# Kernel tuning notes

Measured on AMD Instinct MI355X. Metric: run time of the kernel, lower is better.

## Reference

```python
import jax, jax.numpy as jnp
import numpy as np

# LIDIA core constants (arch_opt.rgb=True => patch_w=5, k=14)
PS = 5          # patch width
K = 14          # number of nearest neighbors
WS = 15         # spatial search window (forward default is 29; 15 keeps working set in ridge regime)
SW = WS // 2    # search radius
PW = PS // 2    # patch radius
RAD = SW + PW   # total reflect pad


def setup_inputs() -> dict:
    key = jax.random.key(0)
    noisy = jax.random.uniform(key, (4, 3, 128, 128), dtype=jnp.float32) * 255.0
    sigma = jnp.full((1,), 25.0, dtype=jnp.float32)  # noise std on 0-255 scale
    return {"noisy": noisy, "sigma": sigma}


def reference(noisy, sigma):
    t, c, h, w = noisy.shape
    # rescale to [-1,1] and remove per-frame means (as in forward)
    x = (noisy / 255.0 - 0.5) / 0.5
    means = x.mean((-2, -1), keepdims=True)
    x = x - means

    # reflect pad so every search offset + patch stays in bounds
    P = jnp.pad(x, ((0, 0), (0, 0), (RAD, RAD), (RAD, RAD)), mode="reflect")
    Hp, Wp = h + 2 * PW, w + 2 * PW
    base = P[:, :, SW:SW + Hp, SW:SW + Wp]  # [t,c,Hp,Wp]

    # --- patch-kNN search: L2 patch distance for every offset in WSxWS window ---
    offs = jnp.stack(jnp.meshgrid(jnp.arange(WS), jnp.arange(WS), indexing="ij"),
                     axis=-1).reshape(-1, 2)  # [WS*WS, 2]

    def energy(o):
        sh = jax.lax.dynamic_slice(P, (0, 0, o[0], o[1]), (t, c, Hp, Wp))
        return ((base - sh) ** 2).sum(1)  # [t,Hp,Wp]

    E = jax.vmap(energy)(offs)  # [WS*WS, t, Hp, Wp] pixel-wise sq diffs

    # box-filter (PSxPS patch sum) -> per-center patch distances
    ones_k = jnp.ones((1, 1, PS, PS), dtype=E.dtype)
    D = jax.lax.conv_general_dilated(E.reshape(-1, 1, Hp, Wp), ones_k,
                                     window_strides=(1, 1), padding="VALID")
    D = D.reshape(WS * WS, t, h, w).transpose(1, 2, 3, 0)  # [t,h,w,WS*WS]

    # top-k smallest distances per query pixel
    negD, idx = jax.lax.top_k(-D, K)  # [t,h,w,K]
    topd = -negD
    oy = idx // WS  # offset row in [0,WS)
    ox = idx % WS

    # --- gather neighbor patches (irregular gather) ---
    # patch top-left in padded coords: row = i + oy  (RAD - SW - PW == 0)
    ii = jnp.arange(h)[None, :, None, None]
    jj = jnp.arange(w)[None, None, :, None]
    r0 = ii + oy  # [t,h,w,K]
    c0 = jj + ox
    a = jnp.arange(PS)
    rows = r0[..., None, None] + a[None, None, None, None, :, None]  # [t,h,w,K,PS,1]
    cols = c0[..., None, None] + a[None, None, None, None, None, :]  # [t,h,w,K,1,PS]
    tt = jnp.arange(t)[:, None, None, None, None, None]
    Pt = P.transpose(0, 2, 3, 1)  # [t,Hpad,Wpad,c]
    patches = Pt[tt, rows, cols]  # [t,h,w,K,PS,PS,c]

    # --- denoise: distance-based softmax aggregation over neighbors ---
    sig = sigma[0] / 255.0 / 0.5  # noise std in normalized units
    denom = 2.0 * (c * PS * PS) * (sig * sig) + 1e-8
    wts = jax.nn.softmax(-topd / denom, axis=-1)  # [t,h,w,K]
    deno_p = jnp.einsum("thwk,thwkpqc->thwpqc", wts, patches)  # [t,h,w,PS,PS,c]

    # --- fold: scatter-add overlapping denoised patches + counts ---
    rf = (jnp.arange(h)[:, None, None, None] + a[None, None, :, None])  # [h,1,PS,1]
    cf = (jnp.arange(w)[None, :, None, None] + a[None, None, None, :])  # [1,w,1,PS]
    tf = jnp.arange(t)[:, None, None, None, None]
    acc = jnp.zeros((t, Hp, Wp, c), dtype=deno_p.dtype)
    cnt = jnp.zeros((t, Hp, Wp, 1), dtype=deno_p.dtype)
    acc = acc.at[tf, rf[None], cf[None]].add(deno_p)
    cnt = cnt.at[tf, rf[None], cf[None]].add(
        jnp.ones((t, h, w, PS, PS, 1), dtype=deno_p.dtype))

    deno = acc / (cnt + 1e-10)
    deno = deno[:, PW:PW + h, PW:PW + w, :].transpose(0, 3, 1, 2)  # [t,c,h,w]
    deno = deno + means
    deno = 255.0 * (deno * 0.5 + 0.5)
    return deno
```

## Files before the change

### kernel.cpp

```cpp
#include <hip/hip_runtime.h>

#define T_ 4
#define C_ 3
#define H_ 128
#define W_ 128
#define PS_ 5
#define K_ 14
#define WS_ 15
#define SW_ 7
#define PW_ 2
#define RAD_ 9
#define HP_ 146
#define NOFF 225
#define NPIX (T_*H_*W_)
#define NQ 2

#define TILE 16
#define SPR 34
#define SPS 35
#define SSR 30
#define SSS 33
#define OB 23
#define CSOG 324

#define AT 8
#define APR 22
#define APS 23
#define AWR 12
#define AWS 20

typedef unsigned int u32;

__device__ __forceinline__ float4 load_refl(const float* __restrict__ noisy,
                                            int t, int py, int px) {
    int ry = py - RAD_; if (ry < 0) ry = -ry; if (ry > H_-1) ry = 2*(H_-1) - ry;
    int rx = px - RAD_; if (rx < 0) rx = -rx; if (rx > W_-1) rx = 2*(W_-1) - rx;
    const float* nt = noisy + (size_t)t*(C_*H_*W_) + ry*W_ + rx;
    float4 v;
    v.x = nt[0]          * (1.0f/127.5f) - 1.0f;
    v.y = nt[H_*W_]      * (1.0f/127.5f) - 1.0f;
    v.z = nt[2*(H_*W_)]  * (1.0f/127.5f) - 1.0f;
    v.w = 0.f;
    return v;
}

__global__ __launch_bounds__(512, 4) void fused_topk(const float* __restrict__ noisy,
                                                     uint4* __restrict__ pkey) {
    __shared__ __align__(16) float4 sP[SPR*SPS];
    __shared__ __align__(16) float  sS[SSR*SSS];
    __shared__ __align__(16) float  cs[OB*CSOG];

    const int tid = threadIdx.x;
    const int pix = tid & 255;
    const int part = tid >> 8;
    const int tx = pix & 15, ty = pix >> 4;
    const int z = blockIdx.z;
    const int t = z >> 1, q = z & 1;
    const int i0 = blockIdx.y * TILE, j0 = blockIdx.x * TILE;

    {
        float* qsq = cs;
        for (int e = tid; e < SPR*SPR; e += 512) {
            int r = e / SPR, c = e % SPR;
            float4 v = load_refl(noisy, t, i0 + r, j0 + c);
            sP[r*SPS + c] = v;
            qsq[r*35 + c] = v.x*v.x + v.y*v.y + v.z*v.z;
        }
    }
    __syncthreads();

    {
        const float* qsq = cs;
        float* cq  = cs + 1200;
        for (int e = tid; e < 30*34; e += 512) {
            int r = e / 34, c = e - r*34;
            const float* qp = &qsq[r*35 + c];
            cq[r*35 + c] = qp[0] + qp[35] + qp[70] + qp[105] + qp[140];
        }
        __syncthreads();
        for (int e = tid; e < 30*30; e += 512) {
            int r = e / 30, c = e - r*30;
            const float* cp = &cq[r*35 + c];
            sS[r*SSS + c] = cp[0] + cp[1] + cp[2] + cp[3] + cp[4];
        }
        __syncthreads();
    }

    const float Sbase = sS[(ty + SW_)*SSS + (tx + SW_)];

    const int og = tid / 20;
    const int cc = tid - og*20;
    const bool p1act = (tid < OB*20);
    float bx[20], by[20], bz[20];
    if (p1act) {
        #pragma unroll
        for (int r = 0; r < 20; ++r) {
            float4 v = sP[(SW_ + r)*SPS + (cc + SW_)];
            bx[r] = v.x; by[r] = v.y; bz[r] = v.z;
        }
    }
    float* myv = &cs[og*CSOG + cc];

    const int p2o = tid >> 4;
    const int p2i = tid & 15;
    float* p2row = &cs[p2o*CSOG + p2i*20];

    const float* vb = &cs[ty*20 + tx];

    u32 kb[K_];
    #pragma unroll
    for (int k = 0; k < K_; ++k) kb[k] = 0xFFFFFFFFu;

    const int obeg = q ? 113 : 0;
    const int oend = q ? 225 : 113;
    const int nb = (oend - obeg + OB - 1) / OB;

    for (int bi = 0; bi < nb; ++bi) {
        const int ob = (q == 0) ? (obeg + (nb - 1 - bi)*OB) : (obeg + bi*OB);
        int o = ob + og;
        if (p1act && o < oend) {
            u32 oyu = (u32)o / 15u, oxu = (u32)o - oyu*15u;
            const float4* sp = &sP[(int)oyu*SPS + cc + (int)oxu];
            float ring[5]; float run = 0.f;
            #pragma unroll
            for (int r = 0; r < 20; ++r) {
                float4 sv = sp[r*SPS];
                float hr = bx[r]*sv.x + by[r]*sv.y + bz[r]*sv.z;
                if (r < 5) run += hr;
                else       run += hr - ring[r % 5];
                ring[r % 5] = hr;
                if (r >= 4) myv[(r-4)*20] = run;
            }
        }
        __syncthreads();
        if (p2o < OB && (ob + p2o) < oend) {
            float4 A = *(const float4*)(p2row);
            float4 B = *(const float4*)(p2row + 4);
            float4 Cv = *(const float4*)(p2row + 8);
            float4 Dv = *(const float4*)(p2row + 12);
            float4 Ev = *(const float4*)(p2row + 16);
            float v0=A.x,v1=A.y,v2=A.z,v3=A.w,v4=B.x,v5=B.y,v6=B.z,v7=B.w;
            float v8=Cv.x,v9=Cv.y,v10=Cv.z,v11=Cv.w,v12=Dv.x,v13=Dv.y,v14=Dv.z,v15=Dv.w;
            float v16=Ev.x,v17=Ev.y,v18=Ev.z,v19=Ev.w;
            float r0 = v0+v1+v2+v3+v4;
            float r1 = r0 + v5 - v0;
            float r2 = r1 + v6 - v1;
            float r3 = r2 + v7 - v2;
            float r4 = r3 + v8 - v3;
            float r5 = r4 + v9 - v4;
            float r6 = r5 + v10 - v5;
            float r7 = r6 + v11 - v6;
            float r8 = r7 + v12 - v7;
            float r9 = r8 + v13 - v8;
            float r10 = r9 + v14 - v9;
            float r11 = r10 + v15 - v10;
            float r12 = r11 + v16 - v11;
            float r13 = r12 + v17 - v12;
            float r14 = r13 + v18 - v13;
            float r15 = r14 + v19 - v14;
            *(float4*)(p2row)      = make_float4(r0, r1, r2, r3);
            *(float4*)(p2row + 4)  = make_float4(r4, r5, r6, r7);
            *(float4*)(p2row + 8)  = make_float4(r8, r9, r10, r11);
            *(float4*)(p2row + 12) = make_float4(r12, r13, r14, r15);
        }
        __syncthreads();
        for (int g = part; g < OB; g += 2) {
            int o2 = ob + g;
            if (o2 >= oend) break;
            u32 oy2 = (u32)o2 / 15u, ox2 = (u32)o2 - oy2*15u;
            float V = vb[g*CSOG];
            float d = fmaxf(Sbase + sS[(ty + (int)oy2)*SSS + (tx + (int)ox2)] - 2.f*V, 0.f);
            u32 c = (__float_as_uint(d) & 0xFFFFFF00u) | (u32)o2;
            #pragma unroll
            for (int k = K_-1; k > 0; --k) kb[k] = min(kb[k], max(kb[k-1], c));
            kb[0] = min(kb[0], c);
        }
        __syncthreads();
    }

    if (part == 1) {
        u32* ex = (u32*)cs + pix*20;
        *(uint4*)(ex)      = make_uint4(kb[0],  kb[1],  kb[2],  kb[3]);
        *(uint4*)(ex + 4)  = make_uint4(kb[4],  kb[5],  kb[6],  kb[7]);
        *(uint4*)(ex + 8)  = make_uint4(kb[8],  kb[9],  kb[10], kb[11]);
        *(uint4*)(ex + 12) = make_uint4(kb[12], kb[13], 0xFFFFFFFFu, 0xFFFFFFFFu);
    }
    __syncthreads();
    if (part == 0) {
        const u32* ex = (const u32*)cs + pix*20;
        uint4 e0 = *(const uint4*)(ex);
        uint4 e1 = *(const uint4*)(ex + 4);
        uint4 e2 = *(const uint4*)(ex + 8);
        uint4 e3 = *(const uint4*)(ex + 12);
        u32 A[16] = {kb[0],kb[1],kb[2],kb[3],kb[4],kb[5],kb[6],kb[7],
                     kb[8],kb[9],kb[10],kb[11],kb[12],kb[13],0xFFFFFFFFu,0xFFFFFFFFu};
        u32 B[16] = {e0.x,e0.y,e0.z,e0.w, e1.x,e1.y,e1.z,e1.w,
                     e2.x,e2.y,e2.z,e2.w, e3.x,e3.y,e3.z,e3.w};
        #pragma unroll
        for (int i2 = 0; i2 < 16; ++i2) A[i2] = min(A[i2], B[15 - i2]);
        #define CEX(x,y) { u32 mn = min(A[x],A[y]); u32 mx = max(A[x],A[y]); A[x]=mn; A[y]=mx; }
        CEX(0,8) CEX(1,9) CEX(2,10) CEX(3,11) CEX(4,12) CEX(5,13) CEX(6,14) CEX(7,15)
        CEX(0,4) CEX(1,5) CEX(2,6) CEX(3,7) CEX(8,12) CEX(9,13) CEX(10,14) CEX(11,15)
        CEX(0,2) CEX(1,3) CEX(4,6) CEX(5,7) CEX(8,10) CEX(9,11) CEX(12,14) CEX(13,15)
        CEX(0,1) CEX(2,3) CEX(4,5) CEX(6,7) CEX(8,9) CEX(10,11) CEX(12,13) CEX(14,15)
        #undef CEX
        int px = ((t*H_ + i0 + ty)*W_ + j0 + tx);
        uint4* pk = pkey + ((size_t)q*NPIX + px)*4;
        pk[0] = make_uint4(A[0],  A[1],  A[2],  A[3]);
        pk[1] = make_uint4(A[4],  A[5],  A[6],  A[7]);
        pk[2] = make_uint4(A[8],  A[9],  A[10], A[11]);
        pk[3] = make_uint4(A[12], A[13], A[14], A[15]);
    }
}

__global__ __launch_bounds__(256, 4) void agg_kernel(const float* __restrict__ noisy,
                                                     const uint4* __restrict__ pkey,
                                                     const float* __restrict__ sigma,
                                                     float* __restrict__ out) {
    __shared__ float sPx[APR*APS];
    __shared__ float sPy[APR*APS];
    __shared__ float sPz[APR*APS];
    __shared__ float sWt[AWR*AWR*AWS];
    __shared__ uint4 sIx[AWR*AWR];

    const int tid = threadIdx.x;
    const int part = tid & 3;
    const int lp = tid >> 2;
    const int tx = lp & 7, ty = lp >> 3;
    const int i0 = blockIdx.y * AT, j0 = blockIdx.x * AT;
    const int t = blockIdx.z;

    for (int e = tid; e < APR*APR; e += 256) {
        int r = e / APR, c = e - r*APR;
        float4 v = load_refl(noisy, t, i0 + 2 + r, j0 + 2 + c);
        sPx[r*APS + c] = v.x;
        sPy[r*APS + c] = v.y;
        sPz[r*APS + c] = v.z;
    }

    if (tid < AWR*AWR) {
        int r = tid / AWR, c = tid - r*AWR;
        int qi = i0 - 2 + r, qj = j0 - 2 + c;
        if (qi >= 0 && qi < H_ && qj >= 0 && qj < W_) {
            size_t px = ((size_t)t*H_ + qi)*W_ + qj;
            u32 A[16];
            {
                const uint4* pk = pkey + px*4;
                uint4 a0=pk[0], a1=pk[1], a2=pk[2], a3=pk[3];
                A[0]=a0.x; A[1]=a0.y; A[2]=a0.z; A[3]=a0.w;
                A[4]=a1.x; A[5]=a1.y; A[6]=a1.z; A[7]=a1.w;
                A[8]=a2.x; A[9]=a2.y; A[10]=a2.z; A[11]=a2.w;
                A[12]=a3.x; A[13]=a3.y; A[14]=a3.z; A[15]=a3.w;
            }
            {
                const uint4* pk = pkey + ((size_t)NPIX + px)*4;
                uint4 b0=pk[0], b1=pk[1], b2=pk[2], b3=pk[3];
                u32 B[16] = {b0.x,b0.y,b0.z,b0.w, b1.x,b1.y,b1.z,b1.w,
                             b2.x,b2.y,b2.z,b2.w, b3.x,b3.y,b3.z,b3.w};
                #pragma unroll
                for (int i2 = 0; i2 < 16; ++i2) A[i2] = min(A[i2], B[15 - i2]);
                #define CEX(x,y) { u32 mn = min(A[x],A[y]); u32 mx = max(A[x],A[y]); A[x]=mn; A[y]=mx; }
                CEX(0,8) CEX(1,9) CEX(2,10) CEX(3,11) CEX(4,12) CEX(5,13) CEX(6,14) CEX(7,15)
                CEX(0,4) CEX(1,5) CEX(2,6) CEX(3,7) CEX(8,12) CEX(9,13) CEX(10,14) CEX(11,15)
                CEX(0,2) CEX(1,3) CEX(4,6) CEX(5,7) CEX(8,10) CEX(9,11) CEX(12,14) CEX(13,15)
                CEX(0,1) CEX(2,3) CEX(4,5) CEX(6,7) CEX(8,9) CEX(10,11) CEX(12,13) CEX(14,15)
                #undef CEX
            }
            float sig = sigma[0] * (1.0f/255.0f) * 2.0f;
            float denom = 2.0f * (float)(C_*PS_*PS_) * (sig*sig) + 1e-8f;
            float d0 = __uint_as_float(A[0] & 0xFFFFFF00u);
            float w[K_]; float sum = 0.f;
            #pragma unroll
            for (int k = 0; k < K_; ++k) {
                float d = __uint_as_float(A[k] & 0xFFFFFF00u);
                w[k] = expf(-(d - d0) / denom); sum += w[k];
            }
            float inv = 1.0f / sum;
            float4* dst = (float4*)&sWt[tid*AWS];
            dst[0] = make_float4(w[0]*inv,  w[1]*inv,  w[2]*inv,  w[3]*inv);
            dst[1] = make_float4(w[4]*inv,  w[5]*inv,  w[6]*inv,  w[7]*inv);
            dst[2] = make_float4(w[8]*inv,  w[9]*inv,  w[10]*inv, w[11]*inv);
            dst[3] = make_float4(w[12]*inv, w[13]*inv, 0.f, 0.f);
            u32 db[K_];
            #pragma unroll
            for (int k = 0; k < K_; ++k) {
                u32 o_ = A[k] & 255u;
                u32 dy = o_ / 15u, dx = o_ - dy*15u;
                db[k] = (dy << 4) | dx;
            }
            uint4 iv;
            iv.x = db[0]  | (db[1]<<8)  | (db[2]<<16)  | (db[3]<<24);
            iv.y = db[4]  | (db[5]<<8)  | (db[6]<<16)  | (db[7]<<24);
            iv.z = db[8]  | (db[9]<<8)  | (db[10]<<16) | (db[11]<<24);
            iv.w = db[12] | (db[13]<<8);
            sIx[tid] = iv;
        }
    }
    __syncthreads();

    const int i = i0 + ty, j = j0 + tx;
    float s0 = 0.f, s1 = 0.f, s2 = 0.f;
    for (int ab = part; ab < 25; ab += 4) {
        int a = ab / 5, b = ab % 5;
        int qi = i + PW_ - a, qj = j + PW_ - b;
        if (qi < 0 || qi >= H_ || qj < 0 || qj >= W_) continue;
        int le = (ty + 4 - a)*AWR + (tx + 4 - b);
        const float4* wv = (const float4*)&sWt[le*AWS];
        float4 wa = wv[0], wb = wv[1], wc = wv[2], wd = wv[3];
        uint4 ip = sIx[le];
        #define ACC(wval, bbits) { \
            u32 b_ = (bbits); \
            int li = (ty + (int)(b_ >> 4))*APS + tx + (int)(b_ & 15u); \
            float w_ = (wval); \
            s0 += w_ * sPx[li]; s1 += w_ * sPy[li]; s2 += w_ * sPz[li]; }
        ACC(wa.x, ip.x & 255u);       ACC(wa.y, (ip.x>>8) & 255u);
        ACC(wa.z, (ip.x>>16) & 255u); ACC(wa.w, ip.x>>24);
        ACC(wb.x, ip.y & 255u);       ACC(wb.y, (ip.y>>8) & 255u);
        ACC(wb.z, (ip.y>>16) & 255u); ACC(wb.w, ip.y>>24);
        ACC(wc.x, ip.z & 255u);       ACC(wc.y, (ip.z>>8) & 255u);
        ACC(wc.z, (ip.z>>16) & 255u); ACC(wc.w, ip.z>>24);
        ACC(wd.x, ip.w & 255u);       ACC(wd.y, (ip.w>>8) & 255u);
        #undef ACC
    }

    s0 += __shfl_xor(s0, 1, 64); s0 += __shfl_xor(s0, 2, 64);
    s1 += __shfl_xor(s1, 1, 64); s1 += __shfl_xor(s1, 2, 64);
    s2 += __shfl_xor(s2, 1, 64); s2 += __shfl_xor(s2, 2, 64);

    if (part == 0) {
        int na = min(4, i + 2) - max(0, i - 125) + 1;
        int nb = min(4, j + 2) - max(0, j - 125) + 1;
        float invc = 1.0f / ((float)(na * nb) + 1e-10f);
        size_t obase = (size_t)t*(C_*H_*W_) + (size_t)i*W_ + j;
        out[obase]             = 127.5f * (s0*invc + 1.0f);
        out[obase +   H_*W_]   = 127.5f * (s1*invc + 1.0f);
        out[obase + 2*(H_*W_)] = 127.5f * (s2*invc + 1.0f);
    }
}

extern "C" void kernel_launch(void* const* d_in, const int* in_sizes, int n_in,
                              void* d_out, int out_size, void* d_ws, size_t ws_size,
                              hipStream_t stream) {
    const float* noisy = (const float*)d_in[0];
    const float* sigma = (const float*)d_in[1];
    float* out = (float*)d_out;
    float* ws  = (float*)d_ws;

    uint4* pkey = (uint4*)ws;

    hipLaunchKernelGGL(fused_topk, dim3(W_/TILE, H_/TILE, T_*NQ), dim3(512), 0, stream,
                       noisy, pkey);

    hipLaunchKernelGGL(agg_kernel, dim3(W_/AT, H_/AT, T_), dim3(256), 0, stream,
                       noisy, pkey, sigma, out);
}
```

Baseline: 57.13 us.

## Software-pipeline the three offset-batch stages with double-buffered shared memory

Restructures the offset-batch loop into a three-stage software pipeline: vertical patch sums for batch i, horizontal sums for batch i-1 and top-k insertion for batch i-2 all run in one iteration, with a single barrier per iteration instead of three. Batches shrink to 12 offsets, the column-sum buffer is double-buffered, and horizontal results go to a separate double-buffered array. The goal is fewer block-wide barriers and more overlap between stages. In exchange, shared memory use grows, which may lower occupancy, and there are more loop iterations, each with fewer active threads per stage.

```diff
diff --git a/kernel.cpp b/kernel.cpp
--- a/kernel.cpp
+++ b/kernel.cpp
@@ -20,8 +20,12 @@
 #define SPS 35
 #define SSR 30
 #define SSS 33
-#define OB 23
+#define OB 12
+#define NB 10
 #define CSOG 324
+#define CSBUF (OB*CSOG)
+#define VOG 256
+#define VBUF (OB*VOG)
 
 #define AT 8
 #define APR 22
@@ -44,11 +48,17 @@
     return v;
 }
 
+__device__ __forceinline__ void batch_of(int q, int bi, int& ob, int& len) {
+    if (q == 0) { int oi = NB-1 - bi; ob = oi*OB; len = (oi == NB-1) ? 5 : OB; }
+    else        { ob = 113 + bi*OB;   len = (bi == NB-1) ? 4 : OB; }
+}
+
 __global__ __launch_bounds__(512, 4) void fused_topk(const float* __restrict__ noisy,
                                                      uint4* __restrict__ pkey) {
     __shared__ __align__(16) float4 sP[SPR*SPS];
     __shared__ __align__(16) float  sS[SSR*SSS];
-    __shared__ __align__(16) float  cs[OB*CSOG];
+    __shared__ __align__(16) float  cs[2*CSBUF];
+    __shared__ __align__(16) float  vb[2*VBUF];
 
     const int tid = threadIdx.x;
     const int pix = tid & 255;
@@ -90,90 +100,93 @@
 
     const int og = tid / 20;
     const int cc = tid - og*20;
-    const bool p1act = (tid < OB*20);
+    const bool p1thr = (tid < OB*20);
     float bx[20], by[20], bz[20];
-    if (p1act) {
+    if (p1thr) {
         #pragma unroll
         for (int r = 0; r < 20; ++r) {
             float4 v = sP[(SW_ + r)*SPS + (cc + SW_)];
             bx[r] = v.x; by[r] = v.y; bz[r] = v.z;
         }
     }
-    float* myv = &cs[og*CSOG + cc];
-
-    const int p2o = tid >> 4;
-    const int p2i = tid & 15;
-    float* p2row = &cs[p2o*CSOG + p2i*20];
-
-    const float* vb = &cs[ty*20 + tx];
+
+    const int t2 = tid - 256;
+    const bool p2thr = (t2 >= 0 && t2 < OB*16);
+    const int p2g = p2thr ? (t2 >> 4) : 0;
+    const int p2i = t2 & 15;
 
     u32 kb[K_];
     #pragma unroll
     for (int k = 0; k < K_; ++k) kb[k] = 0xFFFFFFFFu;
 
-    const int obeg = q ? 113 : 0;
-    const int oend = q ? 225 : 113;
-    const int nb = (oend - obeg + OB - 1) / OB;
-
-    for (int bi = 0; bi < nb; ++bi) {
-        const int ob = (q == 0) ? (obeg + (nb - 1 - bi)*OB) : (obeg + bi*OB);
-        int o = ob + og;
-        if (p1act && o < oend) {
-            u32 oyu = (u32)o / 15u, oxu = (u32)o - oyu*15u;
-            const float4* sp = &sP[(int)oyu*SPS + cc + (int)oxu];
-            float ring[5]; float run = 0.f;
-            #pragma unroll
-            for (int r = 0; r < 20; ++r) {
-                float4 sv = sp[r*SPS];
-                float hr = bx[r]*sv.x + by[r]*sv.y + bz[r]*sv.z;
-                if (r < 5) run += hr;
-                else       run += hr - ring[r % 5];
-                ring[r % 5] = hr;
-                if (r >= 4) myv[(r-4)*20] = run;
-            }
-        }
-        __syncthreads();
-        if (p2o < OB && (ob + p2o) < oend) {
-            float4 A = *(const float4*)(p2row);
-            float4 B = *(const float4*)(p2row + 4);
-            float4 Cv = *(const float4*)(p2row + 8);
-            float4 Dv = *(const float4*)(p2row + 12);
-            float4 Ev = *(const float4*)(p2row + 16);
-            float v0=A.x,v1=A.y,v2=A.z,v3=A.w,v4=B.x,v5=B.y,v6=B.z,v7=B.w;
-            float v8=Cv.x,v9=Cv.y,v10=Cv.z,v11=Cv.w,v12=Dv.x,v13=Dv.y,v14=Dv.z,v15=Dv.w;
-            float v16=Ev.x,v17=Ev.y,v18=Ev.z,v19=Ev.w;
-            float r0 = v0+v1+v2+v3+v4;
-            float r1 = r0 + v5 - v0;
-            float r2 = r1 + v6 - v1;
-            float r3 = r2 + v7 - v2;
-            float r4 = r3 + v8 - v3;
-            float r5 = r4 + v9 - v4;
-            float r6 = r5 + v10 - v5;
-            float r7 = r6 + v11 - v6;
-            float r8 = r7 + v12 - v7;
-            float r9 = r8 + v13 - v8;
-            float r10 = r9 + v14 - v9;
-            float r11 = r10 + v15 - v10;
-            float r12 = r11 + v16 - v11;
-            float r13 = r12 + v17 - v12;
-            float r14 = r13 + v18 - v13;
-            float r15 = r14 + v19 - v14;
-            *(float4*)(p2row)      = make_float4(r0, r1, r2, r3);
-            *(float4*)(p2row + 4)  = make_float4(r4, r5, r6, r7);
-            *(float4*)(p2row + 8)  = make_float4(r8, r9, r10, r11);
-            *(float4*)(p2row + 12) = make_float4(r12, r13, r14, r15);
-        }
-        __syncthreads();
-        for (int g = part; g < OB; g += 2) {
-            int o2 = ob + g;
-            if (o2 >= oend) break;
-            u32 oy2 = (u32)o2 / 15u, ox2 = (u32)o2 - oy2*15u;
-            float V = vb[g*CSOG];
-            float d = fmaxf(Sbase + sS[(ty + (int)oy2)*SSS + (tx + (int)ox2)] - 2.f*V, 0.f);
-            u32 c = (__float_as_uint(d) & 0xFFFFFF00u) | (u32)o2;
-            #pragma unroll
-            for (int k = K_-1; k > 0; --k) kb[k] = min(kb[k], max(kb[k-1], c));
-            kb[0] = min(kb[0], c);
+    for (int i = 0; i <= NB + 1; ++i) {
+        if (i < NB && p1thr) {
+            int ob, len; batch_of(q, i, ob, len);
+            if (og < len) {
+                int o = ob + og;
+                u32 oyu = (u32)o / 15u, oxu = (u32)o - oyu*15u;
+                const float4* sp = &sP[(int)oyu*SPS + cc + (int)oxu];
+                float* myv = &cs[(i & 1)*CSBUF + og*CSOG + cc];
+                float ring[5]; float run = 0.f;
+                #pragma unroll
+                for (int r = 0; r < 20; ++r) {
+                    float4 sv = sp[r*SPS];
+                    float hr = bx[r]*sv.x + by[r]*sv.y + bz[r]*sv.z;
+                    if (r < 5) run += hr;
+                    else       run += hr - ring[r % 5];
+                    ring[r % 5] = hr;
+                    if (r >= 4) myv[(r-4)*20] = run;
+                }
+            }
+        }
+        if (i >= 1 && i <= NB && p2thr) {
+            int ob, len; batch_of(q, i - 1, ob, len);
+            if (p2g < len) {
+                const float* p2row = &cs[((i-1) & 1)*CSBUF + p2g*CSOG + p2i*20];
+                float* vout = &vb[((i-1) & 1)*VBUF + p2g*VOG + p2i*16];
+                float4 A = *(const float4*)(p2row);
+                float4 B = *(const float4*)(p2row + 4);
+                float4 Cv = *(const float4*)(p2row + 8);
+                float4 Dv = *(const float4*)(p2row + 12);
+                float4 Ev = *(const float4*)(p2row + 16);
+                float v0=A.x,v1=A.y,v2=A.z,v3=A.w,v4=B.x,v5=B.y,v6=B.z,v7=B.w;
+                float v8=Cv.x,v9=Cv.y,v10=Cv.z,v11=Cv.w,v12=Dv.x,v13=Dv.y,v14=Dv.z,v15=Dv.w;
+                float v16=Ev.x,v17=Ev.y,v18=Ev.z,v19=Ev.w;
+                float r0 = v0+v1+v2+v3+v4;
+                float r1 = r0 + v5 - v0;
+                float r2 = r1 + v6 - v1;
+                float r3 = r2 + v7 - v2;
+                float r4 = r3 + v8 - v3;
+                float r5 = r4 + v9 - v4;
+                float r6 = r5 + v10 - v5;
+                float r7 = r6 + v11 - v6;
+                float r8 = r7 + v12 - v7;
+                float r9 = r8 + v13 - v8;
+                float r10 = r9 + v14 - v9;
+                float r11 = r10 + v15 - v10;
+                float r12 = r11 + v16 - v11;
+                float r13 = r12 + v17 - v12;
+                float r14 = r13 + v18 - v13;
+                float r15 = r14 + v19 - v14;
+                *(float4*)(vout)      = make_float4(r0, r1, r2, r3);
+                *(float4*)(vout + 4)  = make_float4(r4, r5, r6, r7);
+                *(float4*)(vout + 8)  = make_float4(r8, r9, r10, r11);
+                *(float4*)(vout + 12) = make_float4(r12, r13, r14, r15);
+            }
+        }
+        if (i >= 2) {
+            int ob, len; batch_of(q, i - 2, ob, len);
+            const float* vbase = &vb[((i-2) & 1)*VBUF + pix];
+            for (int g = part; g < len; g += 2) {
+                int o2 = ob + g;
+                u32 oy2 = (u32)o2 / 15u, ox2 = (u32)o2 - oy2*15u;
+                float V = vbase[g*VOG];
+                float d = fmaxf(Sbase + sS[(ty + (int)oy2)*SSS + (tx + (int)ox2)] - 2.f*V, 0.f);
+                u32 c = (__float_as_uint(d) & 0xFFFFFF00u) | (u32)o2;
+                #pragma unroll
+                for (int k = K_-1; k > 0; --k) kb[k] = min(kb[k], max(kb[k-1], c));
+                kb[0] = min(kb[0], c);
+            }
         }
         __syncthreads();
     }
```

After: 55.85 us. 1.02x faster.
